# Performance work log

Measured on AMD Instinct MI355X. Metric: run time of the kernel, lower is better.

Reference implementation:

```python
import jax, jax.numpy as jnp
import numpy as np
from jax import lax

B, L, T = 64, 512, 52  # batch, seq_len, tag_size = target_size + 2


def setup_inputs() -> dict:
    key = jax.random.key(0)
    kf, kt, kl = jax.random.split(key, 3)
    feats = jax.random.normal(kf, (B, L, T), jnp.float32)
    transitions = jax.random.normal(kt, (T, T), jnp.float32) * 0.1
    # __init__ constraints: nothing transitions INTO start tag, nothing OUT of end tag
    transitions = transitions.at[:, T - 2].set(-1000.0).at[T - 1, :].set(-1000.0)
    lengths = jax.random.randint(kl, (B,), L // 2, L + 1)
    mask = (jnp.arange(L)[None, :] < lengths[:, None]).astype(jnp.int32)
    return {"feats": feats, "mask": mask, "transitions": transitions}


def reference(feats, mask, transitions):
    Bv, Lv, Tv = feats.shape
    START, END = Tv - 2, Tv - 1
    # absorb node potentials into edge potentials: scores[t,b,i,j] = feats[b,t,j] + trans[i,j]
    scores = feats.transpose(1, 0, 2)[:, :, None, :] + transitions[None, None, :, :]  # [L,B,T,T]
    lengths = mask.sum(axis=1)            # [B]
    mask_t = mask.T                       # [L,B]
    bidx = jnp.arange(Bv)

    partition0 = scores[0, :, START, :]   # [B,T]

    def step(partition, xs):
        sc, m = xs                        # sc: [B,T,T], m: [B]
        cur = sc + partition[:, :, None]  # max-plus transition
        new_p = cur.max(axis=1)           # [B,T]
        bp = jnp.argmax(cur, axis=1)      # [B,T]
        bp = jnp.where(m[:, None] > 0, bp, 0)  # zero backpointers at padded steps
        return new_p, (new_p, bp)

    _, (parts, bps) = lax.scan(step, partition0, (scores[1:], mask_t[1:]))
    hist = jnp.concatenate([partition0[None], parts], axis=0)      # [L,B,T]

    last_partition = hist[lengths - 1, bidx]                       # [B,T] value at last valid step
    last_values = last_partition[:, :, None] + transitions[None]   # [B,T,T]
    last_bp = jnp.argmax(last_values, axis=1)                      # [B,T]
    pointer0 = last_bp[:, END]                                     # [B] best tag at last position

    back = jnp.concatenate([bps, jnp.zeros((1, Bv, Tv), bps.dtype)], axis=0)  # [L,B,T]
    # insert the final pointer row at each sequence's last valid timestep
    back = back.at[lengths - 1, bidx, :].set(jnp.broadcast_to(pointer0[:, None], (Bv, Tv)))

    def back_step(ptr, bp_t):
        new_ptr = bp_t[bidx, ptr]
        return new_ptr, new_ptr

    _, rev = lax.scan(back_step, pointer0, back[:-1], reverse=True)  # rev[t] = tag at step t
    decode = jnp.concatenate([rev, pointer0[None]], axis=0)          # [L,B]
    return decode.T                                                  # [B,L]
```

## Files before the change

### kernel.cpp

```cpp
#include <hip/hip_runtime.h>

#define BB 64
#define LL 512
#define TT 52
#define START_TAG 50
#define END_TAG 51

__device__ __forceinline__ void lds_barrier() {
    __asm__ __volatile__("s_waitcnt lgkmcnt(0)\n\ts_barrier" ::: "memory");
}

__device__ __forceinline__ unsigned umin32(unsigned a, unsigned b) { return a < b ? a : b; }

__launch_bounds__(256, 1)
__global__ void viterbi_kernel(const float* __restrict__ feats,
                               const int* __restrict__ mask,
                               const float* __restrict__ trans,
                               int* __restrict__ out) {
    const int b    = blockIdx.x;
    const int tid  = threadIdx.x;
    const int lane = tid & 63;
    const int w    = tid >> 6;
    const int wbase = w * 13;

    __shared__ unsigned long long s_part[2][64 * 5 + 8];
    __shared__ unsigned char s_bp[LL * TT];
    __shared__ int s_tags[LL];
    __shared__ unsigned char s_map[8 * 52];
    __shared__ int s_ent[8];

    int partial = 0;
    const int* mrow = mask + b * LL;
    #pragma unroll
    for (int k = 0; k < LL / 64; ++k) partial += mrow[lane + 64 * k];
    #pragma unroll
    for (int off = 32; off >= 1; off >>= 1) partial += __shfl_xor(partial, off, 64);
    const int n = partial;

    float creg[13];
    #pragma unroll
    for (int q = 0; q < 13; ++q)
        creg[q] = (lane < TT) ? trans[(wbase + q) * TT + lane] : 0.0f;
    const float tE = (lane < TT) ? trans[lane * TT + END_TAG] : 0.0f;

    const float* frow = feats + (size_t)b * LL * TT;

    float bestP = (lane < TT) ? (frow[lane] + trans[START_TAG * TT + lane]) : -3.0e38f;

    #pragma unroll
    for (int k = 0; k < LL / 256; ++k) s_tags[tid + 256 * k] = 0;

    const int slot = lane * 5 + w;

    auto step = [&](int t, int buf, float f) {
        float tmp[13];
        #pragma unroll
        for (int q = 0; q < 13; ++q) tmp[q] = f + creg[q];

        float bv[13];
        #pragma unroll
        for (int q = 0; q < 13; ++q) {
            float pq = __int_as_float(__builtin_amdgcn_readlane(__float_as_int(bestP), wbase + q));
            bv[q] = tmp[q] + pq;
        }

        float m0 = fmaxf(fmaxf(bv[0], bv[1]), bv[2]);
        float m1 = fmaxf(fmaxf(bv[3], bv[4]), bv[5]);
        float m2 = fmaxf(fmaxf(bv[6], bv[7]), bv[8]);
        float m3 = fmaxf(fmaxf(bv[9], bv[10]), bv[11]);
        float M  = fmaxf(fmaxf(fmaxf(m0, m1), fmaxf(m2, m3)), bv[12]);

        unsigned kk[13];
        #pragma unroll
        for (int q = 0; q < 13; ++q) {
            unsigned e  = __float_as_uint(bv[q]) ^ __float_as_uint(M);
            unsigned nz = umin32(e, 1u);
            kk[q] = (nz << 6) | (unsigned)q;
        }
        unsigned k0 = umin32(umin32(kk[0], kk[1]), kk[2]);
        unsigned k1 = umin32(umin32(kk[3], kk[4]), kk[5]);
        unsigned k2 = umin32(umin32(kk[6], kk[7]), kk[8]);
        unsigned k3 = umin32(umin32(kk[9], kk[10]), kk[11]);
        unsigned km = umin32(umin32(umin32(k0, k1), umin32(k2, k3)), kk[12]);
        unsigned pidx = (unsigned)wbase + (km & 63u);

        unsigned long long pk = ((unsigned long long)pidx << 32)
                              | (unsigned long long)__float_as_uint(M);
        s_part[buf][slot] = pk;
        lds_barrier();

        unsigned long long p0 = s_part[buf][lane * 5 + 0];
        unsigned long long p1 = s_part[buf][lane * 5 + 1];
        unsigned long long p2 = s_part[buf][lane * 5 + 2];
        unsigned long long p3 = s_part[buf][lane * 5 + 3];
        float v0 = __uint_as_float((unsigned)p0);
        float v1 = __uint_as_float((unsigned)p1);
        float v2 = __uint_as_float((unsigned)p2);
        float v3 = __uint_as_float((unsigned)p3);
        float cv = fmaxf(fmaxf(v0, v1), fmaxf(v2, v3));
        unsigned cb = __float_as_uint(cv);
        unsigned c0 = (umin32(__float_as_uint(v0) ^ cb, 1u) << 6) | (unsigned)(p0 >> 32);
        unsigned c1 = (umin32(__float_as_uint(v1) ^ cb, 1u) << 6) | (unsigned)(p1 >> 32);
        unsigned c2 = (umin32(__float_as_uint(v2) ^ cb, 1u) << 6) | (unsigned)(p2 >> 32);
        unsigned c3 = (umin32(__float_as_uint(v3) ^ cb, 1u) << 6) | (unsigned)(p3 >> 32);
        unsigned ci = umin32(umin32(c0, c1), umin32(c2, c3)) & 63u;

        bestP = cv;
        if (tid < TT) s_bp[t * TT + tid] = (unsigned char)ci;
    };

    float fr[4];
    #pragma unroll
    for (int d = 0; d < 4; ++d) {
        int tt = 1 + d; if (tt > LL - 1) tt = LL - 1;
        fr[d] = (lane < TT) ? frow[tt * TT + lane] : 0.0f;
    }

    int t = 1;
    for (; t + 3 < n; t += 4) {
        #pragma unroll
        for (int d = 0; d < 4; ++d) {
            float f = fr[d];
            int tt = t + d + 4; if (tt > LL - 1) tt = LL - 1;
            fr[d] = (lane < TT) ? frow[tt * TT + lane] : 0.0f;
            step(t + d, d & 1, f);
        }
    }
    for (int d = 0; t < n; ++t, ++d) step(t, d & 1, fr[d]);

    float lv = (lane < TT) ? (bestP + tE) : -3.0e38f;
    int li = lane;
    #pragma unroll
    for (int off = 32; off >= 1; off >>= 1) {
        float ov = __shfl_xor(lv, off, 64);
        int   oi = __shfl_xor(li, off, 64);
        if (ov > lv || (ov == lv && oi < li)) { lv = ov; li = oi; }
    }
    const int ptr0 = li;

    __syncthreads();

    const int W  = n - 1;
    const int Sc = (W + 7) >> 3;
    {
        int v0 = tid;
        int k0 = v0 / 52, y0 = v0 - k0 * 52;
        int v1 = tid + 256;
        bool a1 = (v1 < 416);
        int k1 = a1 ? v1 / 52 : 7, y1 = a1 ? (v1 - k1 * 52) : 0;
        int s0a = k0 * Sc, s1a = min(s0a + Sc, W);
        int s0b = k1 * Sc, s1b = min(s0b + Sc, W);
        int xa = y0, xb = y1;
        for (int s = 0; s < Sc; ++s) {
            int ga = s0a + s, gb = s0b + s;
            if (ga < s1a) xa = s_bp[(n - 1 - ga) * TT + xa];
            if (gb < s1b) xb = s_bp[(n - 1 - gb) * TT + xb];
        }
        s_map[k0 * 52 + y0] = (unsigned char)xa;
        if (a1) s_map[k1 * 52 + y1] = (unsigned char)xb;
    }
    __syncthreads();
    if (tid == 0) {
        int e = ptr0; s_ent[0] = e;
        #pragma unroll
        for (int k = 1; k < 8; ++k) { e = s_map[(k - 1) * 52 + e]; s_ent[k] = e; }
        s_tags[n - 1] = ptr0;
        s_tags[LL - 1] = ptr0;
    }
    __syncthreads();
    if (tid < 8) {
        int k = tid;
        int x = s_ent[k];
        int ss0 = k * Sc, ss1 = min(ss0 + Sc, W);
        for (int s = ss0; s < ss1; ++s) {
            x = s_bp[(n - 1 - s) * TT + x];
            s_tags[n - 2 - s] = x;
        }
    }
    __syncthreads();

    int* orow = out + b * LL;
    #pragma unroll
    for (int k = 0; k < LL / 256; ++k) orow[tid + 256 * k] = s_tags[tid + 256 * k];
}

extern "C" void kernel_launch(void* const* d_in, const int* in_sizes, int n_in,
                              void* d_out, int out_size, void* d_ws, size_t ws_size,
                              hipStream_t stream) {
    const float* feats = (const float*)d_in[0];
    const int*   mask  = (const int*)d_in[1];
    const float* trans = (const float*)d_in[2];
    int* out = (int*)d_out;
    viterbi_kernel<<<dim3(BB), dim3(256), 0, stream>>>(feats, mask, trans, out);
}
```

Before: 289.9 us.

## Defer argmax backpointer computation off the critical max-plus chain

Moves the per-step argmax index computation out of the serial recurrence. Each step now writes only the float max to LDS before the barrier and computes the previous step's local argmax index in its shadow. The cross-wave selection and backpointer store rotate among waves, with one wave per step, instead of being done every step by the threads holding the result. Feature-plus-transition sums are precomputed one step ahead. This shortens the dependent chain per timestep and removes 64-bit LDS traffic, at the cost of extra registers for the previous step's values and an epilogue that finalises the last backpointer.

```diff
diff --git a/kernel.cpp b/kernel.cpp
--- a/kernel.cpp
+++ b/kernel.cpp
@@ -9,7 +9,6 @@
 __device__ __forceinline__ void lds_barrier() {
     __asm__ __volatile__("s_waitcnt lgkmcnt(0)\n\ts_barrier" ::: "memory");
 }
-
 __device__ __forceinline__ unsigned umin32(unsigned a, unsigned b) { return a < b ? a : b; }
 
 __launch_bounds__(256, 1)
@@ -23,7 +22,8 @@
     const int w    = tid >> 6;
     const int wbase = w * 13;
 
-    __shared__ unsigned long long s_part[2][64 * 5 + 8];
+    __shared__ float s_val[2][64 * 5 + 4];
+    __shared__ unsigned char s_idx[2][256];
     __shared__ unsigned char s_bp[LL * TT];
     __shared__ int s_tags[LL];
     __shared__ unsigned char s_map[8 * 52];
@@ -50,83 +50,119 @@
     #pragma unroll
     for (int k = 0; k < LL / 256; ++k) s_tags[tid + 256 * k] = 0;
 
-    const int slot = lane * 5 + w;
-
-    auto step = [&](int t, int buf, float f) {
-        float tmp[13];
-        #pragma unroll
-        for (int q = 0; q < 13; ++q) tmp[q] = f + creg[q];
+    const int vslot = lane * 5 + w;
+
+    float f1 = (lane < TT) ? frow[TT + lane] : 0.0f;
+    float fcur[13];
+    #pragma unroll
+    for (int q = 0; q < 13; ++q) fcur[q] = f1 + creg[q];
+    float fr[4];
+    #pragma unroll
+    for (int d = 0; d < 4; ++d) {
+        int tt = 2 + d; if (tt > LL - 1) tt = LL - 1;
+        fr[d] = (lane < TT) ? frow[tt * TT + lane] : 0.0f;
+    }
+
+    float bvP[13];
+    #pragma unroll
+    for (int q = 0; q < 13; ++q) bvP[q] = 0.0f;
+    float MP = 0.0f;
+    float v0P = 0.0f, v1P = 0.0f, v2P = 0.0f, v3P = 0.0f;
+
+    auto step = [&](int t, int d_ring, int rsel) {
+        const int buf = t & 1;
+        const float Pprev = bestP;
 
         float bv[13];
         #pragma unroll
         for (int q = 0; q < 13; ++q) {
             float pq = __int_as_float(__builtin_amdgcn_readlane(__float_as_int(bestP), wbase + q));
-            bv[q] = tmp[q] + pq;
-        }
-
+            bv[q] = fcur[q] + pq;
+        }
         float m0 = fmaxf(fmaxf(bv[0], bv[1]), bv[2]);
         float m1 = fmaxf(fmaxf(bv[3], bv[4]), bv[5]);
         float m2 = fmaxf(fmaxf(bv[6], bv[7]), bv[8]);
         float m3 = fmaxf(fmaxf(bv[9], bv[10]), bv[11]);
         float M  = fmaxf(fmaxf(fmaxf(m0, m1), fmaxf(m2, m3)), bv[12]);
-
+        s_val[buf][vslot] = M;
+
+        {
+            unsigned mb = __float_as_uint(MP);
+            unsigned kk[13];
+            #pragma unroll
+            for (int q = 0; q < 13; ++q)
+                kk[q] = (umin32(__float_as_uint(bvP[q]) ^ mb, 1u) << 6) | (unsigned)q;
+            unsigned k0 = umin32(umin32(kk[0], kk[1]), kk[2]);
+            unsigned k1 = umin32(umin32(kk[3], kk[4]), kk[5]);
+            unsigned k2 = umin32(umin32(kk[6], kk[7]), kk[8]);
+            unsigned k3 = umin32(umin32(kk[9], kk[10]), kk[11]);
+            unsigned km = umin32(umin32(umin32(k0, k1), umin32(k2, k3)), kk[12]);
+            s_idx[buf ^ 1][(lane << 2) + w] = (unsigned char)(km & 63u);
+        }
+
+        lds_barrier();
+
+        float v0 = s_val[buf][lane * 5 + 0];
+        float v1 = s_val[buf][lane * 5 + 1];
+        float v2 = s_val[buf][lane * 5 + 2];
+        float v3 = s_val[buf][lane * 5 + 3];
+        float nbest = fmaxf(fmaxf(v0, v1), fmaxf(v2, v3));
+
+        if (t >= 2 && w == rsel) {
+            unsigned idx4 = *(const unsigned*)(s_idx[buf ^ 1] + (lane << 2));
+            unsigned cb = __float_as_uint(Pprev);
+            unsigned a0 = (umin32(__float_as_uint(v0P) ^ cb, 1u) << 2) | 0u;
+            unsigned a1 = (umin32(__float_as_uint(v1P) ^ cb, 1u) << 2) | 1u;
+            unsigned a2 = (umin32(__float_as_uint(v2P) ^ cb, 1u) << 2) | 2u;
+            unsigned a3 = (umin32(__float_as_uint(v3P) ^ cb, 1u) << 2) | 3u;
+            unsigned wm = umin32(umin32(a0, a1), umin32(a2, a3)) & 3u;
+            unsigned loc = (idx4 >> (wm << 3)) & 63u;
+            if (lane < TT) s_bp[(t - 1) * TT + lane] = (unsigned char)(wm * 13u + loc);
+        }
+
+        bestP = nbest;
+        #pragma unroll
+        for (int q = 0; q < 13; ++q) bvP[q] = bv[q];
+        MP = M; v0P = v0; v1P = v1; v2P = v2; v3P = v3;
+
+        float fN = fr[d_ring];
+        #pragma unroll
+        for (int q = 0; q < 13; ++q) fcur[q] = fN + creg[q];
+        int tt = t + 5; if (tt > LL - 1) tt = LL - 1;
+        fr[d_ring] = (lane < TT) ? frow[tt * TT + lane] : 0.0f;
+    };
+
+    int t = 1;
+    for (; t + 3 < n; t += 4) {
+        step(t, 0, 0); step(t + 1, 1, 1); step(t + 2, 2, 2); step(t + 3, 3, 3);
+    }
+    for (int d = 0; t < n; ++t, ++d) step(t, d, (t - 1) & 3);
+
+    {
+        unsigned mb = __float_as_uint(MP);
         unsigned kk[13];
         #pragma unroll
-        for (int q = 0; q < 13; ++q) {
-            unsigned e  = __float_as_uint(bv[q]) ^ __float_as_uint(M);
-            unsigned nz = umin32(e, 1u);
-            kk[q] = (nz << 6) | (unsigned)q;
-        }
+        for (int q = 0; q < 13; ++q)
+            kk[q] = (umin32(__float_as_uint(bvP[q]) ^ mb, 1u) << 6) | (unsigned)q;
         unsigned k0 = umin32(umin32(kk[0], kk[1]), kk[2]);
         unsigned k1 = umin32(umin32(kk[3], kk[4]), kk[5]);
         unsigned k2 = umin32(umin32(kk[6], kk[7]), kk[8]);
         unsigned k3 = umin32(umin32(kk[9], kk[10]), kk[11]);
         unsigned km = umin32(umin32(umin32(k0, k1), umin32(k2, k3)), kk[12]);
-        unsigned pidx = (unsigned)wbase + (km & 63u);
-
-        unsigned long long pk = ((unsigned long long)pidx << 32)
-                              | (unsigned long long)__float_as_uint(M);
-        s_part[buf][slot] = pk;
-        lds_barrier();
-
-        unsigned long long p0 = s_part[buf][lane * 5 + 0];
-        unsigned long long p1 = s_part[buf][lane * 5 + 1];
-        unsigned long long p2 = s_part[buf][lane * 5 + 2];
-        unsigned long long p3 = s_part[buf][lane * 5 + 3];
-        float v0 = __uint_as_float((unsigned)p0);
-        float v1 = __uint_as_float((unsigned)p1);
-        float v2 = __uint_as_float((unsigned)p2);
-        float v3 = __uint_as_float((unsigned)p3);
-        float cv = fmaxf(fmaxf(v0, v1), fmaxf(v2, v3));
-        unsigned cb = __float_as_uint(cv);
-        unsigned c0 = (umin32(__float_as_uint(v0) ^ cb, 1u) << 6) | (unsigned)(p0 >> 32);
-        unsigned c1 = (umin32(__float_as_uint(v1) ^ cb, 1u) << 6) | (unsigned)(p1 >> 32);
-        unsigned c2 = (umin32(__float_as_uint(v2) ^ cb, 1u) << 6) | (unsigned)(p2 >> 32);
-        unsigned c3 = (umin32(__float_as_uint(v3) ^ cb, 1u) << 6) | (unsigned)(p3 >> 32);
-        unsigned ci = umin32(umin32(c0, c1), umin32(c2, c3)) & 63u;
-
-        bestP = cv;
-        if (tid < TT) s_bp[t * TT + tid] = (unsigned char)ci;
-    };
-
-    float fr[4];
-    #pragma unroll
-    for (int d = 0; d < 4; ++d) {
-        int tt = 1 + d; if (tt > LL - 1) tt = LL - 1;
-        fr[d] = (lane < TT) ? frow[tt * TT + lane] : 0.0f;
-    }
-
-    int t = 1;
-    for (; t + 3 < n; t += 4) {
-        #pragma unroll
-        for (int d = 0; d < 4; ++d) {
-            float f = fr[d];
-            int tt = t + d + 4; if (tt > LL - 1) tt = LL - 1;
-            fr[d] = (lane < TT) ? frow[tt * TT + lane] : 0.0f;
-            step(t + d, d & 1, f);
-        }
-    }
-    for (int d = 0; t < n; ++t, ++d) step(t, d & 1, fr[d]);
+        s_idx[0][(lane << 2) + w] = (unsigned char)(km & 63u);
+    }
+    __syncthreads();
+    if (w == 0) {
+        unsigned idx4 = *(const unsigned*)(s_idx[0] + (lane << 2));
+        unsigned cb = __float_as_uint(bestP);
+        unsigned a0 = (umin32(__float_as_uint(v0P) ^ cb, 1u) << 2) | 0u;
+        unsigned a1 = (umin32(__float_as_uint(v1P) ^ cb, 1u) << 2) | 1u;
+        unsigned a2 = (umin32(__float_as_uint(v2P) ^ cb, 1u) << 2) | 2u;
+        unsigned a3 = (umin32(__float_as_uint(v3P) ^ cb, 1u) << 2) | 3u;
+        unsigned wm = umin32(umin32(a0, a1), umin32(a2, a3)) & 3u;
+        unsigned loc = (idx4 >> (wm << 3)) & 63u;
+        if (lane < TT) s_bp[(n - 1) * TT + lane] = (unsigned char)(wm * 13u + loc);
+    }
 
     float lv = (lane < TT) ? (bestP + tE) : -3.0e38f;
     int li = lane;
```

Result: slower. 314.2 us (+8.4%).

## Stage feats in double-buffered LDS chunks instead of per-step global prefetch

Applied to the files above, without the earlier changes.

The emission features are now copied cooperatively into two 64-timestep LDS buffers. The Viterbi recurrence reads the next step's features from LDS, replacing the 4-deep register prefetch of global loads inside the serial loop. This aims to take global-memory latency off the critical dependency chain. In exchange it adds about 27KB of LDS, and each new chunk's global-to-LDS copy is issued synchronously at the chunk boundary, which may stall before the stores complete.

```diff
diff --git a/kernel.cpp b/kernel.cpp
--- a/kernel.cpp
+++ b/kernel.cpp
@@ -9,7 +9,6 @@
 __device__ __forceinline__ void lds_barrier() {
     __asm__ __volatile__("s_waitcnt lgkmcnt(0)\n\ts_barrier" ::: "memory");
 }
-
 __device__ __forceinline__ unsigned umin32(unsigned a, unsigned b) { return a < b ? a : b; }
 
 __launch_bounds__(256, 1)
@@ -23,7 +22,8 @@
     const int w    = tid >> 6;
     const int wbase = w * 13;
 
-    __shared__ unsigned long long s_part[2][64 * 5 + 8];
+    __shared__ float s_feat[2][64 * 52 + 64];
+    __shared__ unsigned long long s_part[2][64 * 5 + 4];
     __shared__ unsigned char s_bp[LL * TT];
     __shared__ int s_tags[LL];
     __shared__ unsigned char s_map[8 * 52];
@@ -46,13 +46,25 @@
     const float* frow = feats + (size_t)b * LL * TT;
 
     float bestP = (lane < TT) ? (frow[lane] + trans[START_TAG * TT + lane]) : -3.0e38f;
+    float fcur = (lane < TT) ? frow[TT + lane] : 0.0f;
 
     #pragma unroll
     for (int k = 0; k < LL / 256; ++k) s_tags[tid + 256 * k] = 0;
 
+    #pragma unroll
+    for (int k = 0; k < 13; ++k) {
+        int idx = k * 256 + tid;
+        s_feat[0][idx] = frow[idx];
+        s_feat[1][idx] = frow[64 * 52 + idx];
+    }
+    __syncthreads();
+
     const int slot = lane * 5 + w;
 
-    auto step = [&](int t, int buf, float f) {
+    auto step = [&](int t, float f, float& fnext_out) {
+        int tn = t + 1; if (tn > LL - 1) tn = LL - 1;
+        float fnx = s_feat[(tn >> 6) & 1][(tn & 63) * 52 + lane];
+
         float tmp[13];
         #pragma unroll
         for (int q = 0; q < 13; ++q) tmp[q] = f + creg[q];
@@ -74,8 +86,7 @@
         #pragma unroll
         for (int q = 0; q < 13; ++q) {
             unsigned e  = __float_as_uint(bv[q]) ^ __float_as_uint(M);
-            unsigned nz = umin32(e, 1u);
-            kk[q] = (nz << 6) | (unsigned)q;
+            kk[q] = (umin32(e, 1u) << 6) | (unsigned)q;
         }
         unsigned k0 = umin32(umin32(kk[0], kk[1]), kk[2]);
         unsigned k1 = umin32(umin32(kk[3], kk[4]), kk[5]);
@@ -84,6 +95,7 @@
         unsigned km = umin32(umin32(umin32(k0, k1), umin32(k2, k3)), kk[12]);
         unsigned pidx = (unsigned)wbase + (km & 63u);
 
+        const int buf = t & 1;
         unsigned long long pk = ((unsigned long long)pidx << 32)
                               | (unsigned long long)__float_as_uint(M);
         s_part[buf][slot] = pk;
@@ -107,26 +119,32 @@
 
         bestP = cv;
         if (tid < TT) s_bp[t * TT + tid] = (unsigned char)ci;
+        fnext_out = fnx;
     };
 
-    float fr[4];
-    #pragma unroll
-    for (int d = 0; d < 4; ++d) {
-        int tt = 1 + d; if (tt > LL - 1) tt = LL - 1;
-        fr[d] = (lane < TT) ? frow[tt * TT + lane] : 0.0f;
-    }
-
     int t = 1;
-    for (; t + 3 < n; t += 4) {
-        #pragma unroll
-        for (int d = 0; d < 4; ++d) {
-            float f = fr[d];
-            int tt = t + d + 4; if (tt > LL - 1) tt = LL - 1;
-            fr[d] = (lane < TT) ? frow[tt * TT + lane] : 0.0f;
-            step(t + d, d & 1, f);
-        }
-    }
-    for (int d = 0; t < n; ++t, ++d) step(t, d & 1, fr[d]);
+    for (int c = 0; 64 * c < n; ++c) {
+        if (c >= 1) {
+            int src = 64 * (c + 1);
+            if (src < LL) {
+                const float* sp = frow + src * 52;
+                float* dp = s_feat[(c + 1) & 1];
+                #pragma unroll
+                for (int k = 0; k < 13; ++k) {
+                    int idx = k * 256 + tid;
+                    dp[idx] = sp[idx];
+                }
+            }
+        }
+        int tend = 64 * (c + 1); if (tend > n) tend = n;
+        for (; t + 3 < tend; t += 4) {
+            step(t,     fcur, fcur);
+            step(t + 1, fcur, fcur);
+            step(t + 2, fcur, fcur);
+            step(t + 3, fcur, fcur);
+        }
+        for (; t < tend; ++t) step(t, fcur, fcur);
+    }
 
     float lv = (lane < TT) ? (bestP + tE) : -3.0e38f;
     int li = lane;
```

After: 269.2 us. 1.08x faster.
